# Optimization experiments

Hardware: AMD Instinct MI355X
Metric: run time of the kernel (lower is better)

## Reference

```python
import jax, jax.numpy as jnp
import numpy as np

N = 4096        # nodes
E = 131072      # edges (avg degree 32)
IN = 512        # in_channels
HID = 512       # hidden_channels
HEADS = 4       # GAT heads
LAYERS = 3      # residual GCN layers
G = 16          # graphs in batch
OUT = 1         # out_channels
NEG_SLOPE = 0.2 # GAT LeakyReLU slope


def setup_inputs() -> dict:
    key = jax.random.key(0)
    ks = jax.random.split(key, 9)
    s = 0.02
    x = jax.random.normal(ks[0], (N, IN), dtype=jnp.float32)
    edge_index = jax.random.randint(ks[1], (2, E), 0, N)
    batch = jnp.sort(jax.random.randint(ks[2], (N,), 0, G))
    W_gat = jax.random.normal(ks[3], (HEADS, IN, HID), dtype=jnp.float32) * s
    a_src = jax.random.normal(ks[4], (HEADS, HID), dtype=jnp.float32) * s
    a_dst = jax.random.normal(ks[5], (HEADS, HID), dtype=jnp.float32) * s
    W_gcn = jax.random.normal(ks[6], (LAYERS, HID, HID), dtype=jnp.float32) * s
    fc_w = jax.random.normal(ks[7], (HID, OUT), dtype=jnp.float32) * s
    fc_b = jnp.zeros((OUT,), dtype=jnp.float32)
    return {"x": x, "edge_index": edge_index, "batch": batch,
            "W_gat": W_gat, "a_src": a_src, "a_dst": a_dst,
            "W_gcn": W_gcn, "fc_w": fc_w, "fc_b": fc_b}


def reference(x, edge_index, batch, W_gat, a_src, a_dst, W_gcn, fc_w, fc_b):
    src, dst = edge_index[0], edge_index[1]

    # ---- LatentRelationCapturerGAT: multi-head GAT, one output per head ----
    h = jnp.einsum('nc,hcd->nhd', x, W_gat)                    # [N,H,D]
    lg_src = jnp.einsum('nhd,hd->nh', h, a_src)                # [N,H]
    lg_dst = jnp.einsum('nhd,hd->nh', h, a_dst)                # [N,H]
    e = jax.nn.leaky_relu(lg_src[src] + lg_dst[dst], NEG_SLOPE)  # [E,H]
    # segment softmax over incoming edges of each destination node
    m = jax.ops.segment_max(e, dst, num_segments=N)            # [N,H]
    w = jnp.exp(e - m[dst])                                    # [E,H]
    z = jax.ops.segment_sum(w, dst, num_segments=N)            # [N,H]
    alpha = w / (z[dst] + 1e-16)                               # [E,H]
    H0 = jax.ops.segment_sum(alpha[:, :, None] * h[src], dst, num_segments=N)  # [N,H,D]

    # ---- dense adjacency build + GCN normalization (shared across heads) ----
    A = jnp.zeros((N, N), dtype=x.dtype).at[src, dst].set(1.0)
    A = A + jnp.eye(N, dtype=x.dtype)                          # self-loops
    dinv = jax.lax.rsqrt(jnp.sum(A, axis=1))                   # deg >= 1
    A_hat = dinv[:, None] * A * dinv[None, :]                  # D^-1/2 (A+I) D^-1/2

    # ---- DeepResidualGCN: H <- relu(A_hat @ H @ W_l) + H (heads batched) ----
    H = H0
    for l in range(W_gcn.shape[0]):
        P = jnp.einsum('nm,mhd->nhd', A_hat, H)                # propagate
        H = jax.nn.relu(jnp.einsum('nhd,de->nhe', P, W_gcn[l])) + H

    # ---- per-head global mean pool, then mean over heads ----
    ones = jnp.ones((N,), dtype=x.dtype)
    cnt = jnp.maximum(jax.ops.segment_sum(ones, batch, num_segments=G), 1.0)  # [G]
    pooled = jax.ops.segment_sum(H, batch, num_segments=G) / cnt[:, None, None]  # [G,H,D]
    feats = pooled.mean(axis=1)                                # [G,D]

    return feats @ fc_w + fc_b                                 # [G,OUT]
```

## Files before the change

### kernel.cpp

```cpp
#include <hip/hip_runtime.h>
#include <cstdint>
#include <cstddef>

#define Nn    4096
#define Ee    131072
#define INC   512
#define HIDC  512
#define HEADS 4
#define NLAY  3
#define GG    16
#define FW    2048
#define ALDS  2112
#define BLDS  4160

typedef __attribute__((ext_vector_type(8))) short bfrag;
typedef __attribute__((ext_vector_type(4))) float ffrag;

__device__ __forceinline__ ushort f2bf(float v){
  uint u = __builtin_bit_cast(uint, v);
  u += 0x7fffu + ((u>>16)&1u);
  return (ushort)(u>>16);
}
__device__ __forceinline__ float bf2f(ushort s){
  uint u = ((uint)s)<<16; return __builtin_bit_cast(float, u);
}
__device__ __forceinline__ void fma8(float* acc, uint4 g, float w){
  uint u[4] = {g.x, g.y, g.z, g.w};
  #pragma unroll
  for (int q=0;q<4;q++){
    float lo = __builtin_bit_cast(float, u[q]<<16);
    float hi = __builtin_bit_cast(float, u[q] & 0xffff0000u);
    acc[2*q]   += w*lo;
    acc[2*q+1] += w*hi;
  }
}
__device__ __forceinline__ void pack8(void* p, const float* a){
  uint4 o;
  o.x = (uint)f2bf(a[0]) | ((uint)f2bf(a[1])<<16);
  o.y = (uint)f2bf(a[2]) | ((uint)f2bf(a[3])<<16);
  o.z = (uint)f2bf(a[4]) | ((uint)f2bf(a[5])<<16);
  o.w = (uint)f2bf(a[6]) | ((uint)f2bf(a[7])<<16);
  *(uint4*)p = o;
}
__device__ __forceinline__ uint4 cvt8(float4 a, float4 b){
  uint4 o;
  o.x = (uint)f2bf(a.x) | ((uint)f2bf(a.y)<<16);
  o.y = (uint)f2bf(a.z) | ((uint)f2bf(a.w)<<16);
  o.z = (uint)f2bf(b.x) | ((uint)f2bf(b.y)<<16);
  o.w = (uint)f2bf(b.z) | ((uint)f2bf(b.w)<<16);
  return o;
}

__global__ __launch_bounds__(256) void prep(
    const float* __restrict__ Wgat, ushort* __restrict__ Tgat,
    const float* __restrict__ Wgcn, ushort* __restrict__ Tgcn,
    const int* __restrict__ src, const int* __restrict__ dst,
    int* __restrict__ indeg, unsigned int* __restrict__ bitmap,
    int* __restrict__ cnt_s, int* __restrict__ flag){
  __shared__ float tile[32][33];
  int b = blockIdx.x, t = threadIdx.x;
  if (b < 1792){
    int z = b >> 8, xy = b & 255;
    const float* W; ushort* T; int bb;
    if (z < 4){ W = Wgat; T = Tgat; bb = z; } else { W = Wgcn; T = Tgcn; bb = z-4; }
    int r0 = (xy>>4)*32, c0 = (xy&15)*32;
    int i = t>>3, j0 = (t&7)*4;
    const float* Wb = W + (size_t)bb*512*512;
    float4 v = *(const float4*)(Wb + (size_t)(r0+i)*512 + c0 + j0);
    tile[i][j0]=v.x; tile[i][j0+1]=v.y; tile[i][j0+2]=v.z; tile[i][j0+3]=v.w;
    __syncthreads();
    ushort* o = T + (size_t)bb*512*512 + (size_t)(c0+i)*512 + r0 + j0;
    #pragma unroll
    for (int q=0;q<4;q++) o[q] = f2bf(tile[j0+q][i]);
  } else {
    int e = (b-1792)*256 + t; if (e>=Ee) return;
    int s = src[e], d = dst[e];
    atomicAdd(&indeg[d],1);
    unsigned int key = (unsigned int)s*Nn + (unsigned int)d;
    unsigned int bit = 1u<<(key&31);
    unsigned int old = atomicOr(&bitmap[key>>5], bit);
    int f = (old & bit) ? 0 : 1;
    flag[e] = f;
    if (f) atomicAdd(&cnt_s[s],1);
  }
}

template<bool AF32>
__device__ __forceinline__ void gemm_core(
    const void* __restrict__ Av, const ushort* __restrict__ B,
    const ushort* Res, ushort* Cb,
    int N, int K, int relu_res, int m0, int n0,
    ushort* Ah, ushort* Bh)
{
  int t = threadIdx.x;
  int srA = t>>2, kqA = t&3;
  int wA = (kqA*66 + srA)*8;
  int srB = t>>1, cB = t&1;
  const ushort* pB = B + (size_t)(n0+srB)*K + cB*16;
  int wB0 = ((2*cB)*130 + srB)*8;
  int wB1 = wB0 + 130*8;

  int wave = t>>6, lane = t&63;
  int wm = (wave&1)*32, wn = (wave>>1)*64;
  int lm = lane&15, quad = lane>>4;

  ushort resv[2][4][4];
  if (relu_res){
    #pragma unroll
    for (int mt=0; mt<2; mt++)
      #pragma unroll
      for (int r=0;r<4;r++){
        int grow = m0 + wm + mt*16 + quad*4 + r;
        #pragma unroll
        for (int nt=0; nt<4; nt++){
          int gcol = n0 + wn + nt*16 + lm;
          resv[mt][nt][r] = Res[(size_t)grow*N + gcol];
        }
      }
  }

  ffrag acc[2][4];
  #pragma unroll
  for (int i=0;i<2;i++){
    #pragma unroll
    for (int j=0;j<4;j++) acc[i][j] = (ffrag){0.f,0.f,0.f,0.f};
  }

  const ushort* pA16 = (const ushort*)Av + (size_t)(m0+srA)*K + kqA*8;
  const float*  pA32 = (const float*)Av  + (size_t)(m0+srA)*K + kqA*8;

  uint4 ra; float4 raf0, raf1;
  if (AF32){ raf0 = *(const float4*)(pA32); raf1 = *(const float4*)(pA32+4); }
  else     { ra = *(const uint4*)(pA16); }
  uint4 rb0 = *(const uint4*)(pB);  uint4 rb1 = *(const uint4*)(pB+8);
  *(uint4*)&Ah[wA]  = AF32 ? cvt8(raf0, raf1) : ra;
  *(uint4*)&Bh[wB0] = rb0; *(uint4*)&Bh[wB1] = rb1;
  if (K > 32){
    if (AF32){ raf0 = *(const float4*)(pA32+32); raf1 = *(const float4*)(pA32+36); }
    else     { ra = *(const uint4*)(pA16+32); }
    rb0 = *(const uint4*)(pB+32); rb1 = *(const uint4*)(pB+40);
  }
  __syncthreads();

  for (int k0 = 0; k0 < K; k0 += 32){
    int cur = (k0>>5)&1, nxt = cur^1;
    const ushort* Ac = Ah + cur*ALDS;
    const ushort* Bc = Bh + cur*BLDS;
    bfrag af[2];
    #pragma unroll
    for (int mt=0; mt<2; mt++)
      af[mt] = *(const bfrag*)&Ac[(quad*66 + wm + mt*16 + lm)*8];
    #pragma unroll
    for (int nt=0; nt<4; nt++){
      bfrag bf = *(const bfrag*)&Bc[(quad*130 + wn + nt*16 + lm)*8];
      #pragma unroll
      for (int mt=0; mt<2; mt++)
        acc[mt][nt] = __builtin_amdgcn_mfma_f32_16x16x32_bf16(af[mt], bf, acc[mt][nt], 0,0,0);
    }
    if (k0+32 < K){
      *(uint4*)&Ah[nxt*ALDS + wA]  = AF32 ? cvt8(raf0, raf1) : ra;
      *(uint4*)&Bh[nxt*BLDS + wB0] = rb0; *(uint4*)&Bh[nxt*BLDS + wB1] = rb1;
      if (k0+64 < K){
        if (AF32){ raf0 = *(const float4*)(pA32+k0+64); raf1 = *(const float4*)(pA32+k0+68); }
        else     { ra = *(const uint4*)(pA16+k0+64); }
        rb0 = *(const uint4*)(pB+k0+64); rb1 = *(const uint4*)(pB+k0+72);
      }
    }
    __syncthreads();
  }

  #pragma unroll
  for (int mt=0; mt<2; mt++){
    #pragma unroll
    for (int nt=0; nt<4; nt++){
      #pragma unroll
      for (int r=0;r<4;r++){
        int grow = m0 + wm + mt*16 + quad*4 + r;
        int gcol = n0 + wn + nt*16 + lm;
        size_t off = (size_t)grow*N + gcol;
        float v = acc[mt][nt][r];
        if (relu_res) v = fmaxf(v,0.f) + bf2f(resv[mt][nt][r]);
        Cb[off] = f2bf(v);
      }
    }
  }
}

__global__ __launch_bounds__(256) void gemm_bf(
    const ushort* __restrict__ A, const ushort* __restrict__ B,
    const ushort* Res, ushort* Cb,
    int N, int K, int relu_res)
{
  __shared__ __align__(16) ushort Ah[2*ALDS];
  __shared__ __align__(16) ushort Bh[2*BLDS];
  gemm_core<false>(A, B, Res, Cb, N, K, relu_res,
                   blockIdx.y*64, blockIdx.x*128, Ah, Bh);
}

__global__ __launch_bounds__(256) void gat_gemm_ep2(
    const float* __restrict__ x, const ushort* __restrict__ WgatT, ushort* __restrict__ hbf,
    const int* __restrict__ src, const int* __restrict__ dst, const int* __restrict__ flag,
    const int* __restrict__ rp_d, int* __restrict__ fill_d, int* __restrict__ slist,
    const int* __restrict__ rp_s, int* __restrict__ fill_s, int2* __restrict__ cw,
    const float* __restrict__ dinv)
{
  __shared__ __align__(16) ushort Ah[2*ALDS];
  __shared__ __align__(16) ushort Bh[2*BLDS];
  int b = blockIdx.x;
  if (b < 1024){
    int m0 = (b>>4)*64, n0 = (b&15)*128;
    gemm_core<true>(x, WgatT, nullptr, hbf, FW, INC, 0, m0, n0, Ah, Bh);
  } else {
    int e = (b-1024)*256 + threadIdx.x; if (e>=Ee) return;
    int s = src[e], d = dst[e];
    int p = atomicAdd(&fill_d[d],1); slist[rp_d[d]+p] = s;
    if (flag[e]){
      int q = atomicAdd(&fill_s[s],1);
      cw[rp_s[s]+q] = make_int2(d, __float_as_int(dinv[d]));
    }
  }
}

__global__ __launch_bounds__(256) void compute_lg(const ushort* __restrict__ hbf,
    const float* __restrict__ a_src, const float* __restrict__ a_dst,
    float* __restrict__ lgs, float* __restrict__ lgd){
  int n = blockIdx.x; int t = threadIdx.x;
  int hd = t>>6, lane = t&63;
  uint4 g = *(const uint4*)(hbf + (size_t)n*FW + hd*HIDC + lane*8);
  float h[8] = {0,0,0,0,0,0,0,0};
  fma8(h, g, 1.0f);
  float4 as0 = *(const float4*)(a_src + hd*HIDC + lane*8);
  float4 as1 = *(const float4*)(a_src + hd*HIDC + lane*8 + 4);
  float4 ad0 = *(const float4*)(a_dst + hd*HIDC + lane*8);
  float4 ad1 = *(const float4*)(a_dst + hd*HIDC + lane*8 + 4);
  float s1 = h[0]*as0.x + h[1]*as0.y + h[2]*as0.z + h[3]*as0.w
           + h[4]*as1.x + h[5]*as1.y + h[6]*as1.z + h[7]*as1.w;
  float s2 = h[0]*ad0.x + h[1]*ad0.y + h[2]*ad0.z + h[3]*ad0.w
           + h[4]*ad1.x + h[5]*ad1.y + h[6]*ad1.z + h[7]*ad1.w;
  for (int off=32; off; off>>=1){ s1 += __shfl_down(s1,off); s2 += __shfl_down(s2,off); }
  if (lane==0){ lgs[n*HEADS+hd]=s1; lgd[n*HEADS+hd]=s2; }
}

__global__ __launch_bounds__(1024) void scan3(const int* __restrict__ indeg, int* __restrict__ rp_d,
    const int* __restrict__ cnt_s, int* __restrict__ rp_s, float* __restrict__ dinv,
    const int* __restrict__ batch, int* __restrict__ goff){
  __shared__ int sums[1024];
  __shared__ int cnt2[GG];
  int t = threadIdx.x;
  if (blockIdx.x == 2){
    if (t<GG) cnt2[t]=0;
    __syncthreads();
    for (int i=t;i<Nn;i+=1024) atomicAdd(&cnt2[batch[i]],1);
    __syncthreads();
    if (t==0){ int run=0; for (int g=0; g<GG; g++){ goff[g]=run; run+=cnt2[g]; } goff[GG]=run; }
    return;
  }
  const int* cnt = blockIdx.x ? cnt_s : indeg;
  int* rowptr    = blockIdx.x ? rp_s  : rp_d;
  int v[4]; int s=0;
  #pragma unroll
  for (int i=0;i<4;i++){ int idx=t*4+i; v[i] = cnt[idx]; s+=v[i]; }
  sums[t]=s; __syncthreads();
  for (int off=1; off<1024; off<<=1){
    int other = (t>=off)? sums[t-off] : 0;
    __syncthreads();
    sums[t] += other;
    __syncthreads();
  }
  int run = (t>0)? sums[t-1] : 0;
  #pragma unroll
  for (int i=0;i<4;i++){
    int idx=t*4+i; rowptr[idx]=run; run+=v[i];
    if (blockIdx.x) dinv[idx] = 1.0f/sqrtf((float)(1+v[i]));
  }
  if (t==1023) rowptr[Nn]=sums[1023];
}

__global__ __launch_bounds__(256) void gat_aggregate(const ushort* __restrict__ hbf,
    const float* __restrict__ lgs, const float* __restrict__ lgd,
    const int* __restrict__ rowptr, const int* __restrict__ slist,
    ushort* __restrict__ Hbf){
  __shared__ float alds[4][256];
  int t = threadIdx.x;
  int wv = __builtin_amdgcn_readfirstlane(t>>6);
  int lane = t&63;
  int b = blockIdx.x;
  int hd = __builtin_amdgcn_readfirstlane(b & 3);
  int n = ((b>>2)<<2) + wv;
  int beg = __builtin_amdgcn_readfirstlane(rowptr[n]);
  int end = __builtin_amdgcn_readfirstlane(rowptr[n+1]);
  int deg = end - beg;
  float ldst = lgd[n*HEADS+hd];
  float m_ = -3.4e38f, z_ = 0.f;
  for (int i=lane; i<deg; i+=64){
    int s = slist[beg+i];
    float v = lgs[s*HEADS+hd] + ldst;
    v = v>0.f ? v : 0.2f*v;
    float mn = fmaxf(m_, v);
    z_ = z_*__expf(m_-mn) + __expf(v-mn);
    m_ = mn;
  }
  for (int o=32;o;o>>=1){
    float mo = __shfl_down(m_,o), zo = __shfl_down(z_,o);
    float mn = fmaxf(m_, mo);
    z_ = z_*__expf(m_-mn) + zo*__expf(mo-mn);
    m_ = mn;
  }
  float mx = __shfl(m_,0);
  float zs = __shfl(z_,0);
  float inv = 1.f/(zs+1e-16f);
  float acc[8] = {0,0,0,0,0,0,0,0};
  const ushort* hb = hbf + hd*HIDC + lane*8;
  float* aw = &alds[wv][0];
  for (int base = beg; base < end; base += 256){
    int cn = min(256, end-base);
    for (int i=lane; i<cn; i+=64){
      int s = slist[base+i];
      float v = lgs[s*HEADS+hd] + ldst;
      v = v>0.f ? v : 0.2f*v;
      aw[i] = __expf(v-mx)*inv;
    }
    int c = 0;
    if (c+4 <= cn){
      uint4 g0[4];
      #pragma unroll
      for (int q=0;q<4;q++) g0[q] = *(const uint4*)(hb + (size_t)slist[base+c+q]*FW);
      c += 4;
      for (; c+4<=cn; c+=4){
        uint4 g1[4];
        #pragma unroll
        for (int q=0;q<4;q++) g1[q] = *(const uint4*)(hb + (size_t)slist[base+c+q]*FW);
        #pragma unroll
        for (int q=0;q<4;q++) fma8(acc, g0[q], aw[c-4+q]);
        #pragma unroll
        for (int q=0;q<4;q++) g0[q]=g1[q];
      }
      #pragma unroll
      for (int q=0;q<4;q++) fma8(acc, g0[q], aw[c-4+q]);
    }
    for (; c<cn; c++){
      uint4 g = *(const uint4*)(hb + (size_t)slist[base+c]*FW);
      fma8(acc, g, aw[c]);
    }
  }
  size_t off = (size_t)n*FW + hd*HIDC + lane*8;
  pack8(Hbf + off, acc);
}

__global__ __launch_bounds__(256) void spmm_bf(const ushort* __restrict__ Hbf,
    ushort* __restrict__ Phi,
    const int* __restrict__ rowptr, const int2* __restrict__ cw, const float* __restrict__ dinv){
  int t = threadIdx.x;
  int wv = __builtin_amdgcn_readfirstlane(t>>6);
  int lane = t&63;
  int b = blockIdx.x;
  int ck = __builtin_amdgcn_readfirstlane(b & 3);
  int n = ((b>>2)<<2) + wv;
  int f = (ck<<9) + lane*8;
  float di = dinv[n];
  float acc[8] = {0,0,0,0,0,0,0,0};
  const ushort* hb = Hbf + f;
  uint4 self = *(const uint4*)(hb + (size_t)n*FW);
  fma8(acc, self, di*di);
  int beg = __builtin_amdgcn_readfirstlane(rowptr[n]);
  int end = __builtin_amdgcn_readfirstlane(rowptr[n+1]);
  int i = beg;
  if (i+8 <= end){
    int2 e0[8]; uint4 g0[8];
    #pragma unroll
    for (int q=0;q<8;q++) e0[q] = cw[i+q];
    #pragma unroll
    for (int q=0;q<8;q++) g0[q] = *(const uint4*)(hb + (size_t)e0[q].x*FW);
    i += 8;
    for (; i+8<=end; i+=8){
      int2 e1[8]; uint4 g1[8];
      #pragma unroll
      for (int q=0;q<8;q++) e1[q] = cw[i+q];
      #pragma unroll
      for (int q=0;q<8;q++) g1[q] = *(const uint4*)(hb + (size_t)e1[q].x*FW);
      #pragma unroll
      for (int q=0;q<8;q++) fma8(acc, g0[q], di*__int_as_float(e0[q].y));
      #pragma unroll
      for (int q=0;q<8;q++){ e0[q]=e1[q]; g0[q]=g1[q]; }
    }
    #pragma unroll
    for (int q=0;q<8;q++) fma8(acc, g0[q], di*__int_as_float(e0[q].y));
  }
  for (; i<end; i++){
    int2 e = cw[i];
    uint4 g = *(const uint4*)(hb + (size_t)e.x*FW);
    fma8(acc, g, di*__int_as_float(e.y));
  }
  pack8(Phi + (size_t)n*FW + f, acc);
}

__global__ __launch_bounds__(256) void pool_accum(const ushort* __restrict__ Hb,
    const int* __restrict__ batch, float* __restrict__ psum){
  int d2 = blockIdx.y*256 + threadIdx.x;
  int n0 = blockIdx.x*32;
  int g = batch[n0];
  float s0 = 0.f, s1 = 0.f;
  for (int k=0;k<32;k++){
    int n = n0+k;
    int gn = batch[n];
    if (gn != g){
      atomicAdd(&psum[(size_t)g*FW + d2*2],   s0);
      atomicAdd(&psum[(size_t)g*FW + d2*2+1], s1);
      s0=0.f; s1=0.f; g=gn;
    }
    uint v = *(const uint*)(Hb + (size_t)n*FW + d2*2);
    s0 += bf2f((ushort)(v&0xffff));
    s1 += bf2f((ushort)(v>>16));
  }
  atomicAdd(&psum[(size_t)g*FW + d2*2],   s0);
  atomicAdd(&psum[(size_t)g*FW + d2*2+1], s1);
}
__global__ __launch_bounds__(256) void final_out(const float* __restrict__ psum,
    const int* __restrict__ goff,
    const float* __restrict__ fc_w, const float* __restrict__ fc_b, float* __restrict__ out){
  int g = blockIdx.x; int t = threadIdx.x;
  float cinv = 0.25f / fmaxf((float)(goff[g+1]-goff[g]), 1.f);
  float p = 0.f;
  for (int d=t; d<HIDC; d+=256){
    float f = cinv*(psum[(size_t)g*FW+d] + psum[(size_t)g*FW+HIDC+d]
                  + psum[(size_t)g*FW+2*HIDC+d] + psum[(size_t)g*FW+3*HIDC+d]);
    p += f*fc_w[d];
  }
  __shared__ float red[4];
  for (int off=32; off; off>>=1) p += __shfl_down(p,off);
  if ((t&63)==0) red[t>>6]=p;
  __syncthreads();
  if (t==0) out[g] = red[0]+red[1]+red[2]+red[3] + fc_b[0];
}

extern "C" void kernel_launch(void* const* d_in, const int* in_sizes, int n_in,
                              void* d_out, int out_size, void* d_ws, size_t ws_size,
                              hipStream_t stream){
  const float* x      = (const float*)d_in[0];
  const int*   ei     = (const int*)d_in[1];
  const int*   batch  = (const int*)d_in[2];
  const float* W_gat  = (const float*)d_in[3];
  const float* a_src  = (const float*)d_in[4];
  const float* a_dst  = (const float*)d_in[5];
  const float* W_gcn  = (const float*)d_in[6];
  const float* fc_w   = (const float*)d_in[7];
  const float* fc_b   = (const float*)d_in[8];
  float* out = (float*)d_out;
  const int* src = ei;
  const int* dst = ei + Ee;

  char* w = (char*)d_ws;
  size_t off = 0;
  auto alloc = [&](size_t bytes)->char*{ char* p = w + off; off = (off + bytes + 255) & ~(size_t)255; return p; };
  ushort* hbf    = (ushort*)alloc((size_t)Nn*FW*2);
  ushort* Hbf    = (ushort*)alloc((size_t)Nn*FW*2);
  ushort* WgatT  = (ushort*)alloc((size_t)HEADS*INC*HIDC*2);
  ushort* WgcnT  = (ushort*)alloc((size_t)NLAY*HIDC*HIDC*2);
  float* lgs    = (float*)alloc((size_t)Nn*HEADS*4);
  float* lgd    = (float*)alloc((size_t)Nn*HEADS*4);
  int* indeg    = (int*)alloc(Nn*4);
  int* fill_d   = (int*)alloc(Nn*4);
  int* cnt_s    = (int*)alloc(Nn*4);
  int* fill_s   = (int*)alloc(Nn*4);
  float* psum   = (float*)alloc((size_t)GG*FW*4);
  unsigned int* bitmap = (unsigned int*)alloc((size_t)Nn*Nn/8);
  size_t zero_bytes = (size_t)Nn*4*4 + (size_t)GG*FW*4 + (size_t)Nn*Nn/8;
  int* rowptr_d = (int*)alloc((Nn+1)*4);
  int* slist    = (int*)alloc(Ee*4);
  int* rowptr_s = (int*)alloc((Nn+1)*4);
  int2* cwlist  = (int2*)alloc((size_t)Ee*8);
  int* flag     = (int*)alloc(Ee*4);
  float* dinv   = (float*)alloc(Nn*4);
  int* goff     = (int*)alloc((GG+1)*4);
  ushort* Phi   = hbf;

  hipMemsetAsync(indeg, 0, zero_bytes, stream);

  prep<<<2304,256,0,stream>>>(W_gat, WgatT, W_gcn, WgcnT,
                              src, dst, indeg, bitmap, cnt_s, flag);

  scan3<<<3,1024,0,stream>>>(indeg, rowptr_d, cnt_s, rowptr_s, dinv, batch, goff);

  gat_gemm_ep2<<<1536,256,0,stream>>>(x, WgatT, hbf,
      src, dst, flag, rowptr_d, fill_d, slist, rowptr_s, fill_s, cwlist, dinv);

  compute_lg<<<Nn,256,0,stream>>>(hbf, a_src, a_dst, lgs, lgd);
  gat_aggregate<<<Nn,256,0,stream>>>(hbf, lgs, lgd, rowptr_d, slist, Hbf);

  for (int l=0;l<NLAY;l++){
    spmm_bf<<<Nn,256,0,stream>>>(Hbf, Phi, rowptr_s, cwlist, dinv);
    gemm_bf<<<dim3(HIDC/128, (Nn*HEADS)/64),256,0,stream>>>(Phi,
        WgcnT + (size_t)l*HIDC*HIDC,
        Hbf, Hbf, HIDC, HIDC, 1);
  }

  pool_accum<<<dim3(Nn/32, FW/512),256,0,stream>>>(Hbf, batch, psum);
  final_out<<<GG,256,0,stream>>>(psum, goff, fc_w, fc_b, out);
}
```

Baseline: 342.1 us.

## Fuse GCN layers, pooling and output into one cooperative persistent kernel

Replaces the eight separate launches for the three spmm/gemm layer pairs, pooling and the final output with a single cooperative kernel of 1024 blocks, using grid-wide syncs between stages. The aim is to remove per-launch overhead and tail idle time between the small dependent kernels. It requires four resident blocks per CU and falls back to the old launch sequence otherwise. Grid syncs add their own cost, and the fixed 1024-block grid may balance the spmm work less evenly than 4096 blocks did.

```diff
diff --git a/kernel.cpp b/kernel.cpp
--- a/kernel.cpp
+++ b/kernel.cpp
@@ -1,6 +1,9 @@
 #include <hip/hip_runtime.h>
+#include <hip/hip_cooperative_groups.h>
 #include <cstdint>
 #include <cstddef>
+
+namespace cg = cooperative_groups;
 
 #define Nn    4096
 #define Ee    131072
@@ -347,15 +350,14 @@
   pack8(Hbf + off, acc);
 }
 
-__global__ __launch_bounds__(256) void spmm_bf(const ushort* __restrict__ Hbf,
+__device__ __forceinline__ void spmm_task(const ushort* __restrict__ Hbf,
     ushort* __restrict__ Phi,
-    const int* __restrict__ rowptr, const int2* __restrict__ cw, const float* __restrict__ dinv){
-  int t = threadIdx.x;
+    const int* __restrict__ rowptr, const int2* __restrict__ cw, const float* __restrict__ dinv,
+    int vb, int t){
   int wv = __builtin_amdgcn_readfirstlane(t>>6);
   int lane = t&63;
-  int b = blockIdx.x;
-  int ck = __builtin_amdgcn_readfirstlane(b & 3);
-  int n = ((b>>2)<<2) + wv;
+  int ck = __builtin_amdgcn_readfirstlane(vb & 3);
+  int n = ((vb>>2)<<2) + wv;
   int f = (ck<<9) + lane*8;
   float di = dinv[n];
   float acc[8] = {0,0,0,0,0,0,0,0};
@@ -394,10 +396,15 @@
   pack8(Phi + (size_t)n*FW + f, acc);
 }
 
-__global__ __launch_bounds__(256) void pool_accum(const ushort* __restrict__ Hb,
-    const int* __restrict__ batch, float* __restrict__ psum){
-  int d2 = blockIdx.y*256 + threadIdx.x;
-  int n0 = blockIdx.x*32;
+__global__ __launch_bounds__(256) void spmm_bf(const ushort* __restrict__ Hbf,
+    ushort* __restrict__ Phi,
+    const int* __restrict__ rowptr, const int2* __restrict__ cw, const float* __restrict__ dinv){
+  spmm_task(Hbf, Phi, rowptr, cw, dinv, blockIdx.x, threadIdx.x);
+}
+
+__device__ __forceinline__ void pool_task(const ushort* __restrict__ Hb,
+    const int* __restrict__ batch, float* __restrict__ psum, int xblk, int d2){
+  int n0 = xblk*32;
   int g = batch[n0];
   float s0 = 0.f, s1 = 0.f;
   for (int k=0;k<32;k++){
@@ -415,10 +422,14 @@
   atomicAdd(&psum[(size_t)g*FW + d2*2],   s0);
   atomicAdd(&psum[(size_t)g*FW + d2*2+1], s1);
 }
-__global__ __launch_bounds__(256) void final_out(const float* __restrict__ psum,
+__global__ __launch_bounds__(256) void pool_accum(const ushort* __restrict__ Hb,
+    const int* __restrict__ batch, float* __restrict__ psum){
+  pool_task(Hb, batch, psum, blockIdx.x, blockIdx.y*256 + threadIdx.x);
+}
+__device__ __forceinline__ void final_task(const float* __restrict__ psum,
     const int* __restrict__ goff,
-    const float* __restrict__ fc_w, const float* __restrict__ fc_b, float* __restrict__ out){
-  int g = blockIdx.x; int t = threadIdx.x;
+    const float* __restrict__ fc_w, const float* __restrict__ fc_b, float* __restrict__ out,
+    int g, int t, float* red){
   float cinv = 0.25f / fmaxf((float)(goff[g+1]-goff[g]), 1.f);
   float p = 0.f;
   for (int d=t; d<HIDC; d+=256){
@@ -426,11 +437,49 @@
                   + psum[(size_t)g*FW+2*HIDC+d] + psum[(size_t)g*FW+3*HIDC+d]);
     p += f*fc_w[d];
   }
-  __shared__ float red[4];
   for (int off=32; off; off>>=1) p += __shfl_down(p,off);
   if ((t&63)==0) red[t>>6]=p;
   __syncthreads();
   if (t==0) out[g] = red[0]+red[1]+red[2]+red[3] + fc_b[0];
+}
+__global__ __launch_bounds__(256) void final_out(const float* __restrict__ psum,
+    const int* __restrict__ goff,
+    const float* __restrict__ fc_w, const float* __restrict__ fc_b, float* __restrict__ out){
+  __shared__ float red[4];
+  final_task(psum, goff, fc_w, fc_b, out, blockIdx.x, threadIdx.x, red);
+}
+
+__global__ __launch_bounds__(256,4) void gcn_coop(
+    ushort* __restrict__ Hbf, ushort* __restrict__ Phi,
+    const int* __restrict__ rowptr, const int2* __restrict__ cw, const float* __restrict__ dinv,
+    const ushort* __restrict__ WgcnT,
+    const int* __restrict__ batch, float* __restrict__ psum, const int* __restrict__ goff,
+    const float* __restrict__ fc_w, const float* __restrict__ fc_b, float* __restrict__ out)
+{
+  __shared__ __align__(16) ushort Ah[2*ALDS];
+  __shared__ __align__(16) ushort Bh[2*BLDS];
+  __shared__ float red[4];
+  cg::grid_group grid = cg::this_grid();
+  int b = blockIdx.x, t = threadIdx.x;
+  for (int l=0;l<NLAY;l++){
+    for (int vb = b; vb < Nn; vb += 1024)
+      spmm_task(Hbf, Phi, rowptr, cw, dinv, vb, t);
+    __threadfence();
+    grid.sync();
+    {
+      int n0 = (b&3)*128, m0 = (b>>2)*64;
+      gemm_core<false>(Phi, WgcnT + (size_t)l*HIDC*HIDC, Hbf, Hbf,
+                       HIDC, HIDC, 1, m0, n0, Ah, Bh);
+    }
+    __threadfence();
+    grid.sync();
+  }
+  if (b < 512)
+    pool_task(Hbf, batch, psum, b & 127, (b>>7)*256 + t);
+  __threadfence();
+  grid.sync();
+  if (b < GG)
+    final_task(psum, goff, fc_w, fc_b, out, b, t, red);
 }
 
 extern "C" void kernel_launch(void* const* d_in, const int* in_sizes, int n_in,
@@ -487,13 +536,21 @@
   compute_lg<<<Nn,256,0,stream>>>(hbf, a_src, a_dst, lgs, lgd);
   gat_aggregate<<<Nn,256,0,stream>>>(hbf, lgs, lgd, rowptr_d, slist, Hbf);
 
-  for (int l=0;l<NLAY;l++){
-    spmm_bf<<<Nn,256,0,stream>>>(Hbf, Phi, rowptr_s, cwlist, dinv);
-    gemm_bf<<<dim3(HIDC/128, (Nn*HEADS)/64),256,0,stream>>>(Phi,
-        WgcnT + (size_t)l*HIDC*HIDC,
-        Hbf, Hbf, HIDC, HIDC, 1);
-  }
-
-  pool_accum<<<dim3(Nn/32, FW/512),256,0,stream>>>(Hbf, batch, psum);
-  final_out<<<GG,256,0,stream>>>(psum, goff, fc_w, fc_b, out);
-}
+  int maxB = 0;
+  hipOccupancyMaxActiveBlocksPerMultiprocessor(&maxB, (const void*)gcn_coop, 256, 0);
+  if (maxB >= 4){
+    void* args[] = { (void*)&Hbf, (void*)&Phi, (void*)&rowptr_s, (void*)&cwlist,
+                     (void*)&dinv, (void*)&WgcnT, (void*)&batch, (void*)&psum,
+                     (void*)&goff, (void*)&fc_w, (void*)&fc_b, (void*)&out };
+    hipLaunchCooperativeKernel((void*)gcn_coop, dim3(1024), dim3(256), args, 0, stream);
+  } else {
+    for (int l=0;l<NLAY;l++){
+      spmm_bf<<<Nn,256,0,stream>>>(Hbf, Phi, rowptr_s, cwlist, dinv);
+      gemm_bf<<<dim3(HIDC/128, (Nn*HEADS)/64),256,0,stream>>>(Phi,
+          WgcnT + (size_t)l*HIDC*HIDC,
+          Hbf, Hbf, HIDC, HIDC, 1);
+    }
+    pool_accum<<<dim3(Nn/32, FW/512),256,0,stream>>>(Hbf, batch, psum);
+    final_out<<<GG,256,0,stream>>>(psum, goff, fc_w, fc_b, out);
+  }
+}
```

Result: no change. 342.9 us (+0.2%).
